# Optimization experiments

Measured on AMD Instinct MI355X. Metric: run time of the kernel, lower is better.

The kernel has to match this reference:

```python
import jax, jax.numpy as jnp
import numpy as np

N_WIRES = 4
# Fixed instantiation of tq.RandomLayer(n_ops=8): 5 parameterized rotations + 3 CNOTs
RL_OPS = [("ry", 0), ("rx", 1), ("rz", 2), ("cnot", (0, 1)), ("ry", 3), ("cnot", (2, 3)), ("rx", 0), ("cnot", (1, 2))]


def _rot(state, theta, wire, kind):
    # state: (N,2,2,2,2) complex64; theta: scalar or (N,)
    ax = wire + 1
    s = jnp.moveaxis(state, ax, -1)
    half = jnp.asarray(theta) * 0.5
    c = jnp.cos(half).astype(jnp.complex64)
    sn = jnp.sin(half).astype(jnp.complex64)
    if c.ndim > 0:
        bshape = c.shape + (1,) * (s.ndim - 1 - c.ndim)
        c = c.reshape(bshape)
        sn = sn.reshape(bshape)
    s0, s1 = s[..., 0], s[..., 1]
    if kind == "ry":
        n0, n1 = c * s0 - sn * s1, sn * s0 + c * s1
    elif kind == "rx":
        n0, n1 = c * s0 - 1j * sn * s1, -1j * sn * s0 + c * s1
    else:  # rz
        n0, n1 = (c - 1j * sn) * s0, (c + 1j * sn) * s1
    return jnp.moveaxis(jnp.stack([n0, n1], axis=-1), -1, ax)


def _cnot(state, ctrl, tgt):
    ca, ta = ctrl + 1, tgt + 1
    s = jnp.moveaxis(state, (ca, ta), (-2, -1))
    s = jnp.concatenate([s[..., 0:1, :], s[..., 1:2, ::-1]], axis=-2)
    return jnp.moveaxis(s, (-2, -1), (ca, ta))


def _random_layer(state, params):
    pi = 0
    for op in RL_OPS:
        if op[0] == "cnot":
            state = _cnot(state, op[1][0], op[1][1])
        else:
            state = _rot(state, params[pi], op[1], op[0])
            pi += 1
    return state


def _init_state(n):
    # |0000> for n parallel circuits
    s = jnp.zeros((n, 16), dtype=jnp.complex64).at[:, 0].set(1.0)
    return s.reshape(n, 2, 2, 2, 2)


def _encode_ry(state, angles):
    # angles: (N, 4) -> RY(angle_w) on wire w (tq.GeneralEncoder after reset)
    for w in range(N_WIRES):
        state = _rot(state, angles[:, w], w, "ry")
    return state


def _measure_z(state):
    # <Z_w> for each wire; wire 0 is the most significant axis (tq convention)
    p = state.real ** 2 + state.imag ** 2
    outs = []
    for w in range(N_WIRES):
        axes = tuple(a for a in range(1, 5) if a != w + 1)
        m = p.sum(axis=axes)
        outs.append(m[:, 0] - m[:, 1])
    return jnp.stack(outs, axis=1)


def _forward(x, filter_params, attn_params, kernel_params, W, b):
    B = x.shape[0]
    img = x.reshape(B, 28, 28)
    # 2x2 patches: [(r,c),(r,c+1),(r+1,c),(r+1,c+1)] per patch -> (B*196, 4)
    patches = img.reshape(B, 14, 2, 14, 2).transpose(0, 1, 3, 2, 4).reshape(B * 196, 4)
    # QuantumFilter on all 196 patches in parallel (encoder resets state each call)
    st = _encode_ry(_init_state(B * 196), patches)
    st = _random_layer(st, filter_params)
    features = _measure_z(st).reshape(B, 196 * N_WIRES)  # (B, 784)
    # QuantumSelfAttention: GeneralEncoder only consumes the first 4 features
    st2 = _encode_ry(_init_state(B), features[:, :N_WIRES])
    st2 = _random_layer(st2, attn_params)
    attn_out = _measure_z(st2)  # (B, 4)
    # QuantumKernel: fixed ansatz applied twice to |0000>; |<0000|psi>| (data-independent)
    st3 = _random_layer(_random_layer(_init_state(1), kernel_params), kernel_params)
    k = jnp.abs(st3.reshape(16)[0])
    kernel_out = jnp.broadcast_to(k, (B, 1))
    combined = jnp.concatenate([attn_out, kernel_out], axis=-1)  # (B, 5)
    logits = combined @ W.T + b
    return jax.nn.log_softmax(logits, axis=-1)


def setup_inputs() -> dict:
    key = jax.random.key(0)
    ks = jax.random.split(key, 6)
    B = 4096
    two_pi = 2.0 * np.pi
    return {
        "x": jax.random.normal(ks[0], (B, 28, 28), dtype=jnp.float32),
        "filter_params": jax.random.uniform(ks[1], (5,), dtype=jnp.float32, minval=0.0, maxval=two_pi),
        "attn_params": jax.random.uniform(ks[2], (5,), dtype=jnp.float32, minval=0.0, maxval=two_pi),
        "kernel_params": jax.random.uniform(ks[3], (5,), dtype=jnp.float32, minval=0.0, maxval=two_pi),
        "W": jax.random.normal(ks[4], (10, 5), dtype=jnp.float32) * 0.3,
        "b": jnp.zeros((10,), dtype=jnp.float32),
    }


def reference(x, filter_params, attn_params, kernel_params, W, b):
    return _forward(x, filter_params, attn_params, kernel_params, W, b)
```

## Files before the change

kernel.cpp:

```cpp
#include <hip/hip_runtime.h>
#include <math.h>


#define DEVFN static __device__ __forceinline__


template <int WIRE, int KIND>
DEVFN void rot(float* re, float* im, float half) {
    const float c = __cosf(half) * 0.0f + cosf(half);
    const float s = sinf(half);
    constexpr int bit = 1 << (3 - WIRE);
#pragma unroll
    for (int i = 0; i < 16; ++i) {
        if (i & bit) continue;
        const int j = i | bit;
        const float r0 = re[i], i0 = im[i];
        const float r1 = re[j], i1 = im[j];
        if (KIND == 0) {
            re[i] = c * r0 - s * r1;  im[i] = c * i0 - s * i1;
            re[j] = s * r0 + c * r1;  im[j] = s * i0 + c * i1;
        } else if (KIND == 1) {
            re[i] = c * r0 + s * i1;  im[i] = c * i0 - s * r1;
            re[j] = c * r1 + s * i0;  im[j] = c * i1 - s * r0;
        } else {
            re[i] = c * r0 + s * i0;  im[i] = c * i0 - s * r0;
            re[j] = c * r1 - s * i1;  im[j] = c * i1 + s * r1;
        }
    }
}

template <int C, int T>
DEVFN void cnot(float* re, float* im) {
    constexpr int cb = 1 << (3 - C);
    constexpr int tb = 1 << (3 - T);
#pragma unroll
    for (int i = 0; i < 16; ++i) {
        if ((i & cb) && !(i & tb)) {
            const int j = i | tb;
            const float tr = re[i], ti = im[i];
            re[i] = re[j]; im[i] = im[j];
            re[j] = tr;    im[j] = ti;
        }
    }
}

template <int WIRE>
DEVFN float measZ(const float* re, const float* im) {
    constexpr int bit = 1 << (3 - WIRE);
    float acc = 0.0f;
#pragma unroll
    for (int i = 0; i < 16; ++i) {
        const float p = re[i] * re[i] + im[i] * im[i];
        acc += (i & bit) ? -p : p;
    }
    return acc;
}

DEVFN void init_state(float* re, float* im) {
#pragma unroll
    for (int i = 0; i < 16; ++i) { re[i] = 0.0f; im[i] = 0.0f; }
    re[0] = 1.0f;
}

DEVFN void encode_ry(float* re, float* im, float a0, float a1, float a2, float a3) {
    rot<0, 0>(re, im, a0 * 0.5f);
    rot<1, 0>(re, im, a1 * 0.5f);
    rot<2, 0>(re, im, a2 * 0.5f);
    rot<3, 0>(re, im, a3 * 0.5f);
}

DEVFN void random_layer(float* re, float* im,
                        float p0, float p1, float p2, float p3, float p4) {
    rot<0, 0>(re, im, p0 * 0.5f);
    rot<1, 1>(re, im, p1 * 0.5f);
    rot<2, 2>(re, im, p2 * 0.5f);
    cnot<0, 1>(re, im);
    rot<3, 0>(re, im, p3 * 0.5f);
    cnot<2, 3>(re, im);
    rot<0, 1>(re, im, p4 * 0.5f);
    cnot<1, 2>(re, im);
}

__global__ void __launch_bounds__(256)
quanv_collapsed_kernel(const float* __restrict__ x,
                       const float* __restrict__ fp,
                       const float* __restrict__ ap,
                       const float* __restrict__ kp,
                       const float* __restrict__ W,
                       const float* __restrict__ bia,
                       float* __restrict__ out,
                       int B) {
    const int t = blockIdx.x * blockDim.x + threadIdx.x;
    if (t >= B) return;

    const float* img = x + (size_t)t * 784;
    const float a0 = img[0];
    const float a1 = img[1];
    const float a2 = img[28];
    const float a3 = img[29];

    const float f0 = fp[0], f1 = fp[1], f2 = fp[2], f3 = fp[3], f4 = fp[4];
    const float q0 = ap[0], q1 = ap[1], q2 = ap[2], q3 = ap[3], q4 = ap[4];
    const float k0 = kp[0], k1 = kp[1], k2 = kp[2], k3 = kp[3], k4 = kp[4];

    float re[16], im[16];

    init_state(re, im);
    encode_ry(re, im, a0, a1, a2, a3);
    random_layer(re, im, f0, f1, f2, f3, f4);
    const float m0 = measZ<0>(re, im);
    const float m1 = measZ<1>(re, im);
    const float m2 = measZ<2>(re, im);
    const float m3 = measZ<3>(re, im);

    init_state(re, im);
    encode_ry(re, im, m0, m1, m2, m3);
    random_layer(re, im, q0, q1, q2, q3, q4);
    const float at0 = measZ<0>(re, im);
    const float at1 = measZ<1>(re, im);
    const float at2 = measZ<2>(re, im);
    const float at3 = measZ<3>(re, im);

    init_state(re, im);
    random_layer(re, im, k0, k1, k2, k3, k4);
    random_layer(re, im, k0, k1, k2, k3, k4);
    const float kval = sqrtf(re[0] * re[0] + im[0] * im[0]);

    float logit[10];
    float mx = -INFINITY;
#pragma unroll
    for (int c = 0; c < 10; ++c) {
        float v = bia[c];
        v += at0 * W[c * 5 + 0];
        v += at1 * W[c * 5 + 1];
        v += at2 * W[c * 5 + 2];
        v += at3 * W[c * 5 + 3];
        v += kval * W[c * 5 + 4];
        logit[c] = v;
        mx = fmaxf(mx, v);
    }
    float sum = 0.0f;
#pragma unroll
    for (int c = 0; c < 10; ++c) sum += expf(logit[c] - mx);
    const float lse = logf(sum) + mx;

    float* o = out + (size_t)t * 10;
#pragma unroll
    for (int c = 0; c < 10; ++c) o[c] = logit[c] - lse;
}

extern "C" void kernel_launch(void* const* d_in, const int* in_sizes, int n_in,
                              void* d_out, int out_size, void* d_ws, size_t ws_size,
                              hipStream_t stream) {
    const float* x  = (const float*)d_in[0];
    const float* fp = (const float*)d_in[1];
    const float* ap = (const float*)d_in[2];
    const float* kp = (const float*)d_in[3];
    const float* W  = (const float*)d_in[4];
    const float* b  = (const float*)d_in[5];
    float* out = (float*)d_out;

    const int B = in_sizes[0] / 784;
    const int block = 256;
    const int grid = (B + block - 1) / block;
    quanv_collapsed_kernel<<<grid, block, 0, stream>>>(x, fp, ap, kp, W, b, out, B);
}
```

Measured before the change: 75.10 us.

## Use fast sincos/exp/log intrinsics, hoist parameter trig, vectorize pixel loads, shrink blocks

Replaces the accurate cosf/sinf calls with __sincosf and precomputes the cosine/sine of the 15 shared parameters once per thread instead of once per rotation. It also switches to fast __expf/__logf in the log-softmax, loads the four pixels as two float2 values, and shrinks the block size from 256 to 64. With B=4096 that gives 64 blocks instead of 16, spreading the work over more compute units. The cost is lower-precision transcendentals and a reliance on the float2 loads being 8-byte aligned.

```diff
diff --git a/kernel.cpp b/kernel.cpp
--- a/kernel.cpp
+++ b/kernel.cpp
@@ -6,9 +6,7 @@
 
 
 template <int WIRE, int KIND>
-DEVFN void rot(float* re, float* im, float half) {
-    const float c = __cosf(half) * 0.0f + cosf(half);
-    const float s = sinf(half);
+DEVFN void rot_cs(float* re, float* im, float c, float s) {
     constexpr int bit = 1 << (3 - WIRE);
 #pragma unroll
     for (int i = 0; i < 16; ++i) {
@@ -27,6 +25,13 @@
             re[j] = c * r1 - s * i1;  im[j] = c * i1 + s * r1;
         }
     }
+}
+
+template <int WIRE, int KIND>
+DEVFN void rot(float* re, float* im, float half) {
+    float s, c;
+    __sincosf(half, &s, &c);
+    rot_cs<WIRE, KIND>(re, im, c, s);
 }
 
 template <int C, int T>
@@ -69,19 +74,18 @@
     rot<3, 0>(re, im, a3 * 0.5f);
 }
 
-DEVFN void random_layer(float* re, float* im,
-                        float p0, float p1, float p2, float p3, float p4) {
-    rot<0, 0>(re, im, p0 * 0.5f);
-    rot<1, 1>(re, im, p1 * 0.5f);
-    rot<2, 2>(re, im, p2 * 0.5f);
+DEVFN void random_layer_cs(float* re, float* im, const float* c, const float* s) {
+    rot_cs<0, 0>(re, im, c[0], s[0]);
+    rot_cs<1, 1>(re, im, c[1], s[1]);
+    rot_cs<2, 2>(re, im, c[2], s[2]);
     cnot<0, 1>(re, im);
-    rot<3, 0>(re, im, p3 * 0.5f);
+    rot_cs<3, 0>(re, im, c[3], s[3]);
     cnot<2, 3>(re, im);
-    rot<0, 1>(re, im, p4 * 0.5f);
+    rot_cs<0, 1>(re, im, c[4], s[4]);
     cnot<1, 2>(re, im);
 }
 
-__global__ void __launch_bounds__(256)
+__global__ void __launch_bounds__(64)
 quanv_collapsed_kernel(const float* __restrict__ x,
                        const float* __restrict__ fp,
                        const float* __restrict__ ap,
@@ -94,20 +98,22 @@
     if (t >= B) return;
 
     const float* img = x + (size_t)t * 784;
-    const float a0 = img[0];
-    const float a1 = img[1];
-    const float a2 = img[28];
-    const float a3 = img[29];
+    const float2 p01 = *reinterpret_cast<const float2*>(img);
+    const float2 p23 = *reinterpret_cast<const float2*>(img + 28);
 
-    const float f0 = fp[0], f1 = fp[1], f2 = fp[2], f3 = fp[3], f4 = fp[4];
-    const float q0 = ap[0], q1 = ap[1], q2 = ap[2], q3 = ap[3], q4 = ap[4];
-    const float k0 = kp[0], k1 = kp[1], k2 = kp[2], k3 = kp[3], k4 = kp[4];
+    float fc[5], fs[5], qc[5], qs[5], kc[5], ks[5];
+#pragma unroll
+    for (int i = 0; i < 5; ++i) {
+        __sincosf(fp[i] * 0.5f, &fs[i], &fc[i]);
+        __sincosf(ap[i] * 0.5f, &qs[i], &qc[i]);
+        __sincosf(kp[i] * 0.5f, &ks[i], &kc[i]);
+    }
 
     float re[16], im[16];
 
     init_state(re, im);
-    encode_ry(re, im, a0, a1, a2, a3);
-    random_layer(re, im, f0, f1, f2, f3, f4);
+    encode_ry(re, im, p01.x, p01.y, p23.x, p23.y);
+    random_layer_cs(re, im, fc, fs);
     const float m0 = measZ<0>(re, im);
     const float m1 = measZ<1>(re, im);
     const float m2 = measZ<2>(re, im);
@@ -115,15 +121,15 @@
 
     init_state(re, im);
     encode_ry(re, im, m0, m1, m2, m3);
-    random_layer(re, im, q0, q1, q2, q3, q4);
+    random_layer_cs(re, im, qc, qs);
     const float at0 = measZ<0>(re, im);
     const float at1 = measZ<1>(re, im);
     const float at2 = measZ<2>(re, im);
     const float at3 = measZ<3>(re, im);
 
     init_state(re, im);
-    random_layer(re, im, k0, k1, k2, k3, k4);
-    random_layer(re, im, k0, k1, k2, k3, k4);
+    random_layer_cs(re, im, kc, ks);
+    random_layer_cs(re, im, kc, ks);
     const float kval = sqrtf(re[0] * re[0] + im[0] * im[0]);
 
     float logit[10];
@@ -141,8 +147,8 @@
     }
     float sum = 0.0f;
 #pragma unroll
-    for (int c = 0; c < 10; ++c) sum += expf(logit[c] - mx);
-    const float lse = logf(sum) + mx;
+    for (int c = 0; c < 10; ++c) sum += __expf(logit[c] - mx);
+    const float lse = __logf(sum) + mx;
 
     float* o = out + (size_t)t * 10;
 #pragma unroll
@@ -161,7 +167,7 @@
     float* out = (float*)d_out;
 
     const int B = in_sizes[0] / 784;
-    const int block = 256;
+    const int block = 64;
     const int grid = (B + block - 1) / block;
     quanv_collapsed_kernel<<<grid, block, 0, stream>>>(x, fp, ap, kp, W, b, out, B);
 }
```

After: 69.15 us. -7.9%, faster.
